# Kernel tuning notes

Measured on AMD Instinct MI355X. Metric: run time of the kernel, lower is better.

The kernel has to match this reference:

```python
import jax, jax.numpy as jnp
import numpy as np

B, C, H, N = 2, 128, 128, 2048   # batch, in_channels, hidden_dim, points per view
TEMP = 0.1
ITERS = 20
EPS = 1e-8


def setup_inputs() -> dict:
    key = jax.random.key(0)
    ks = jax.random.split(key, 4)
    s = lambda fan_in: 1.0 / np.sqrt(fan_in)
    return {
        "feat_d": jax.random.normal(ks[0], (B, C, N), jnp.float32),
        "feat_s": jax.random.normal(ks[1], (B, C, N), jnp.float32),
        # dustbin_head params: Conv1d(C->H, k=1) -> ReLU -> Conv1d(H->1, k=1)
        "W1": jax.random.normal(ks[2], (H, C), jnp.float32) * s(C),
        "b1": jnp.zeros((H,), jnp.float32),
        "W2": jax.random.normal(ks[3], (1, H), jnp.float32) * s(H),
        "b2": jnp.zeros((1,), jnp.float32),
    }


def _dustbin_head(x, W1, b1, W2, b2):
    # 1x1 Conv1d == channel matmul. x: [B, C, N] -> [B, 1, N]
    h = jax.nn.relu(jnp.einsum('hc,bcn->bhn', W1, x) + b1[None, :, None])
    return jnp.einsum('oh,bhn->bon', W2, h) + b2[None, :, None]


def _log_cross_view_ot(feat_q, feat_k, dustbin, temperature, iters):
    # scores: [B, Nq, Nk]; dustbin appended as the last row -> [B, Nq+1, Nk]
    scores = jnp.einsum('bcn,bcm->bnm', feat_q, feat_k) / temperature
    log_T0 = jnp.concatenate([scores, dustbin], axis=1)

    def step(log_T, _):
        log_T = log_T - jax.nn.logsumexp(log_T, axis=2, keepdims=True)  # row norm
        log_T = log_T - jax.nn.logsumexp(log_T, axis=1, keepdims=True)  # col norm
        return log_T, None

    log_T, _ = jax.lax.scan(step, log_T0, None, length=iters)
    return log_T


def reference(feat_d, feat_s, W1, b1, W2, b2):
    # N_d == N_s, so the torch F.interpolate calls are identity ops.
    dust_d = _dustbin_head(feat_d, W1, b1, W2, b2)  # [B, 1, N]
    dust_s = _dustbin_head(feat_s, W1, b1, W2, b2)  # [B, 1, N]

    log_T_ds = _log_cross_view_ot(feat_d, feat_s, dust_d, TEMP, ITERS)
    log_T_sd = _log_cross_view_ot(feat_s, feat_d, dust_s, TEMP, ITERS)

    T_ds = jnp.exp(log_T_ds[:, :-1, :])  # drop dustbin row -> [B, N, N]
    T_sd = jnp.exp(log_T_sd[:, :-1, :])

    loss_consistency = jnp.mean((T_ds - jnp.swapaxes(T_sd, 1, 2)) ** 2)

    entropy_ds = -(T_ds * jnp.log(T_ds + EPS)).sum(axis=(1, 2)).mean()
    entropy_sd = -(T_sd * jnp.log(T_sd + EPS)).sum(axis=(1, 2)).mean()
    loss_entropy = 0.5 * (entropy_ds + entropy_sd)

    return loss_consistency + 0.01 * loss_entropy
```

## Files before the change

kernel.cpp:

```cpp
#include <hip/hip_runtime.h>
#include <hip/hip_fp16.h>
#include <math.h>

#define NPTS 2048
#define NB 2
#define NC 128
#define NH 128
#define INV_TEMP 10.0f
#define NITERS 20
#define EPSF 1e-8f

static __device__ __forceinline__ void lse_merge(float& m, float& s, float m2, float s2){
  float M = fmaxf(m, m2);
  s = s * __expf(m - M) + s2 * __expf(m2 - M);
  m = M;
}

static __device__ __forceinline__ void unpack8(uint4 raw, float* x){
  float2 f;
  f = __half22float2(*(__half2*)&raw.x); x[0]=f.x; x[1]=f.y;
  f = __half22float2(*(((__half2*)&raw.x)+1)); x[2]=f.x; x[3]=f.y;
  f = __half22float2(*(__half2*)&raw.z); x[4]=f.x; x[5]=f.y;
  f = __half22float2(*(((__half2*)&raw.z)+1)); x[6]=f.x; x[7]=f.y;
}

static __device__ __forceinline__ float reduce32_lse(float* x){
  float mt[16];
  #pragma unroll
  for (int i = 0; i < 16; ++i) mt[i] = fmaxf(x[i], x[i + 16]);
  #pragma unroll
  for (int st = 8; st >= 1; st >>= 1)
    #pragma unroll
    for (int i = 0; i < 8; ++i) if (i < st) mt[i] = fmaxf(mt[i], mt[i + st]);
  float m = mt[0];
  float s0 = 0.f, s1 = 0.f, s2 = 0.f, s3 = 0.f;
  #pragma unroll
  for (int i = 0; i < 32; i += 4){
    s0 += __expf(x[i]     - m);
    s1 += __expf(x[i + 1] - m);
    s2 += __expf(x[i + 2] - m);
    s3 += __expf(x[i + 3] - m);
  }
  float s = (s0 + s1) + (s2 + s3);
  #pragma unroll
  for (int d = 1; d < 64; d <<= 1){
    float m2 = __shfl_xor(m, d);
    float sx = __shfl_xor(s, d);
    lse_merge(m, s, m2, sx);
  }
  return m + __logf(s);
}

__global__ __launch_bounds__(128) void dust_kernel(
    const float* __restrict__ fd, const float* __restrict__ fs,
    const float* __restrict__ W1, const float* __restrict__ b1,
    const float* __restrict__ W2, const float* __restrict__ b2,
    float* __restrict__ dust_d, float* __restrict__ dust_s){
  const int chunk = blockIdx.x, b = blockIdx.y, view = blockIdx.z;
  const float* x = (view == 0 ? fd : fs) + (size_t)b * NC * NPTS;
  float* out = (view == 0 ? dust_d : dust_s) + (size_t)b * NPTS;
  const int n0 = chunk * 16;
  __shared__ float xs[NC][17];
  __shared__ float red[NH][17];
  const int j = threadIdx.x;
  #pragma unroll
  for (int p = 0; p < 16; ++p) xs[j][p] = x[(size_t)j * NPTS + n0 + p];
  __syncthreads();
  float acc[16];
  float bb = b1[j];
  #pragma unroll
  for (int p = 0; p < 16; ++p) acc[p] = bb;
  for (int c = 0; c < NC; ++c){
    float w = W1[j * NC + c];
    #pragma unroll
    for (int p = 0; p < 16; ++p) acc[p] = fmaf(w, xs[c][p], acc[p]);
  }
  float w2 = W2[j];
  #pragma unroll
  for (int p = 0; p < 16; ++p) red[j][p] = w2 * fmaxf(acc[p], 0.0f);
  __syncthreads();
  for (int s = NH / 2; s >= 1; s >>= 1){
    if (j < s){
      #pragma unroll
      for (int p = 0; p < 16; ++p) red[j][p] += red[j + s][p];
    }
    __syncthreads();
  }
  if (j < 16) out[n0 + j] = red[0][j] + b2[0];
}

#define GP 68
#define KC 64
__global__ __launch_bounds__(256) void gemm_kernel(
    const float* __restrict__ fd, const float* __restrict__ fs,
    __half* __restrict__ S, __half* __restrict__ ST){
  const int cb = blockIdx.x, rb = blockIdx.y, b = blockIdx.z;
  const float* A = fd + (size_t)b * NC * NPTS;
  const float* Bm = fs + (size_t)b * NC * NPTS;
  __shared__ float Als[KC * GP];
  __shared__ float Bls[KC * GP];
  const int tid = threadIdx.x;
  const int tx = tid & 15, ty = tid >> 4;
  float acc[4][4] = {};
  for (int kc = 0; kc < NC; kc += KC){
    for (int idx = tid; idx < KC * 64; idx += 256){
      int ch = idx >> 6, i = idx & 63;
      Als[ch * GP + i] = A[(size_t)(kc + ch) * NPTS + rb * 64 + i];
      Bls[ch * GP + i] = Bm[(size_t)(kc + ch) * NPTS + cb * 64 + i];
    }
    __syncthreads();
    for (int c = 0; c < KC; ++c){
      float4 a4 = *(const float4*)&Als[c * GP + ty * 4];
      float4 b4 = *(const float4*)&Bls[c * GP + tx * 4];
      float av[4] = {a4.x, a4.y, a4.z, a4.w};
      float bv[4] = {b4.x, b4.y, b4.z, b4.w};
      #pragma unroll
      for (int i = 0; i < 4; ++i)
        #pragma unroll
        for (int jj = 0; jj < 4; ++jj)
          acc[i][jj] = fmaf(av[i], bv[jj], acc[i][jj]);
    }
    __syncthreads();
  }
  __half* Sb = S + (size_t)b * NPTS * NPTS;
  __half* STb = ST + (size_t)b * NPTS * NPTS;
  const int r0 = rb * 64 + ty * 4, c0 = cb * 64 + tx * 4;
  #pragma unroll
  for (int i = 0; i < 4; ++i){
    __half2 p[2];
    p[0] = __float22half2_rn(make_float2(acc[i][0]*INV_TEMP, acc[i][1]*INV_TEMP));
    p[1] = __float22half2_rn(make_float2(acc[i][2]*INV_TEMP, acc[i][3]*INV_TEMP));
    *(uint2*)&Sb[(size_t)(r0 + i) * NPTS + c0] = *(uint2*)p;
  }
  #pragma unroll
  for (int jj = 0; jj < 4; ++jj){
    __half2 p[2];
    p[0] = __float22half2_rn(make_float2(acc[0][jj]*INV_TEMP, acc[1][jj]*INV_TEMP));
    p[1] = __float22half2_rn(make_float2(acc[2][jj]*INV_TEMP, acc[3][jj]*INV_TEMP));
    *(uint2*)&STb[(size_t)(c0 + jj) * NPTS + r0] = *(uint2*)p;
  }
}

__global__ __launch_bounds__(512, 4) void phase_kernel(
    const __half* __restrict__ S, const __half* __restrict__ ST,
    const float* __restrict__ dust_d, const float* __restrict__ dust_s,
    float* __restrict__ u_ds, float* __restrict__ u_sd,
    float* __restrict__ v_ds, float* __restrict__ v_sd,
    const int mode){
  const int b = blockIdx.y, mat = blockIdx.z;
  const int w = threadIdx.x >> 6, lane = threadIdx.x & 63;
  const int r = blockIdx.x * 8 + w;
  const int rmax = (mode == 0) ? (NPTS + 1) : NPTS;
  if (blockIdx.x * 8 >= rmax) return;

  __shared__ float lds_off[NPTS];
  {
    const float* off;
    if (mode == 0) off = (mat == 0 ? v_ds : v_sd) + b * NPTS;
    else           off = (mat == 0 ? u_sd : u_ds) + b * (NPTS + 1);
    *(float4*)&lds_off[threadIdx.x * 4] = *(const float4*)&off[threadIdx.x * 4];
  }
  __syncthreads();

  if (r >= rmax) return;

  float x[32];
  if (mode == 0 && r == NPTS){
    const float* drow = (mat == 0 ? dust_d : dust_s) + b * NPTS;
    #pragma unroll
    for (int k = 0; k < 8; ++k){
      const int c = (k * 64 + lane) * 4;
      float4 rv = *(const float4*)&drow[c];
      float4 o  = *(const float4*)&lds_off[c];
      x[k*4+0]=rv.x+o.x; x[k*4+1]=rv.y+o.y; x[k*4+2]=rv.z+o.z; x[k*4+3]=rv.w+o.w;
    }
  } else {
    const __half* row = (mat == 0 ? S : ST) + ((size_t)b * NPTS + r) * NPTS;
    #pragma unroll
    for (int k2 = 0; k2 < 4; ++k2){
      const int c = (k2 * 64 + lane) * 8;
      uint4 raw = *(const uint4*)&row[c];
      float xr[8];
      unpack8(raw, xr);
      float4 o0 = *(const float4*)&lds_off[c];
      float4 o1 = *(const float4*)&lds_off[c + 4];
      x[k2*8+0]=xr[0]+o0.x; x[k2*8+1]=xr[1]+o0.y; x[k2*8+2]=xr[2]+o0.z; x[k2*8+3]=xr[3]+o0.w;
      x[k2*8+4]=xr[4]+o1.x; x[k2*8+5]=xr[5]+o1.y; x[k2*8+6]=xr[6]+o1.z; x[k2*8+7]=xr[7]+o1.w;
    }
  }

  float lse = reduce32_lse(x);
  if (lane == 0){
    if (mode == 0){
      (mat == 0 ? u_ds : u_sd)[b * (NPTS + 1) + r] = -lse;
    } else {
      float dsc = (mat == 0 ? dust_s : dust_d)[b * NPTS + r];
      float uN  = (mat == 0 ? u_sd : u_ds)[b * (NPTS + 1) + NPTS];
      float e = dsc + uN;
      float M2 = fmaxf(lse, e);
      lse = M2 + __logf(__expf(lse - M2) + __expf(e - M2));
      (mat == 0 ? v_sd : v_ds)[b * NPTS + r] = -lse;
    }
  }
}

__global__ __launch_bounds__(512, 4) void loss_kernel(
    const __half* __restrict__ S,
    const float* __restrict__ u_ds, const float* __restrict__ u_sd,
    const float* __restrict__ v_ds, const float* __restrict__ v_sd,
    float* __restrict__ part){
  const int b = blockIdx.y;
  const int w = threadIdx.x >> 6, lane = threadIdx.x & 63;
  const int r = blockIdx.x * 8 + w;

  __shared__ float lds_vds[NPTS];
  __shared__ float lds_usd[NPTS];
  *(float4*)&lds_vds[threadIdx.x * 4] = *(const float4*)&v_ds[b * NPTS + threadIdx.x * 4];
  *(float4*)&lds_usd[threadIdx.x * 4] = *(const float4*)&u_sd[b * (NPTS + 1) + threadIdx.x * 4];
  __syncthreads();

  const __half* row = S + ((size_t)b * NPTS + r) * NPTS;
  const float uds = u_ds[b * (NPTS + 1) + r];
  const float vsd = v_sd[b * NPTS + r];
  float sd = 0.f, e1 = 0.f, e2 = 0.f;
  #pragma unroll
  for (int k2 = 0; k2 < 4; ++k2){
    const int c = (k2 * 64 + lane) * 8;
    uint4 raw = *(const uint4*)&row[c];
    float sv[8];
    unpack8(raw, sv);
    float4 a0 = *(const float4*)&lds_vds[c];
    float4 a1 = *(const float4*)&lds_vds[c + 4];
    float4 q0 = *(const float4*)&lds_usd[c];
    float4 q1 = *(const float4*)&lds_usd[c + 4];
    float av[8] = {a0.x,a0.y,a0.z,a0.w,a1.x,a1.y,a1.z,a1.w};
    float qv[8] = {q0.x,q0.y,q0.z,q0.w,q1.x,q1.y,q1.z,q1.w};
    #pragma unroll
    for (int i = 0; i < 8; ++i){
      float t1 = __expf(sv[i] + uds + av[i]);
      float t2 = __expf(sv[i] + qv[i] + vsd);
      float d = t1 - t2;
      sd += d * d;
      e1 += t1 * __logf(t1 + EPSF);
      e2 += t2 * __logf(t2 + EPSF);
    }
  }
  #pragma unroll
  for (int d = 1; d < 64; d <<= 1){
    sd += __shfl_xor(sd, d);
    e1 += __shfl_xor(e1, d);
    e2 += __shfl_xor(e2, d);
  }
  if (lane == 0){
    float* p = part + ((size_t)b * NPTS + r) * 4;
    p[0] = sd; p[1] = e1; p[2] = e2;
  }
}

__global__ __launch_bounds__(256) void final_kernel(const float* __restrict__ part, float* __restrict__ out){
  const int tid = threadIdx.x;
  float s0 = 0.f, s1 = 0.f, s2 = 0.f;
  for (int i = tid; i < NB * NPTS; i += 256){
    s0 += part[(size_t)i * 4 + 0];
    s1 += part[(size_t)i * 4 + 1];
    s2 += part[(size_t)i * 4 + 2];
  }
  #pragma unroll
  for (int d = 1; d < 64; d <<= 1){
    s0 += __shfl_xor(s0, d);
    s1 += __shfl_xor(s1, d);
    s2 += __shfl_xor(s2, d);
  }
  __shared__ float rs[4][3];
  const int w = tid >> 6;
  if ((tid & 63) == 0){ rs[w][0] = s0; rs[w][1] = s1; rs[w][2] = s2; }
  __syncthreads();
  if (tid == 0){
    float a0 = rs[0][0] + rs[1][0] + rs[2][0] + rs[3][0];
    float a1 = rs[0][1] + rs[1][1] + rs[2][1] + rs[3][1];
    float a2 = rs[0][2] + rs[1][2] + rs[2][2] + rs[3][2];
    float lc = a0 / (float)((size_t)NB * NPTS * NPTS);
    float le = -0.5f * (a1 + a2) / (float)NB;
    out[0] = lc + 0.01f * le;
  }
}

extern "C" void kernel_launch(void* const* d_in, const int* in_sizes, int n_in,
                              void* d_out, int out_size, void* d_ws, size_t ws_size,
                              hipStream_t stream){
  const float* fd = (const float*)d_in[0];
  const float* fs = (const float*)d_in[1];
  const float* W1 = (const float*)d_in[2];
  const float* b1 = (const float*)d_in[3];
  const float* W2 = (const float*)d_in[4];
  const float* b2 = (const float*)d_in[5];
  char* ws = (char*)d_ws;
  __half* S  = (__half*)ws;
  __half* ST = S + (size_t)NB * NPTS * NPTS;
  float* fws = (float*)(ws + 2 * sizeof(__half) * (size_t)NB * NPTS * NPTS);
  float* dust_d = fws;
  float* dust_s = dust_d + (size_t)NB * NPTS;
  float* u_ds   = dust_s + (size_t)NB * NPTS;
  float* u_sd   = u_ds + (size_t)NB * (NPTS + 1);
  float* v_ds   = u_sd + (size_t)NB * (NPTS + 1);
  float* v_sd   = v_ds + (size_t)NB * NPTS;
  float* part   = v_sd + (size_t)NB * NPTS;

  hipMemsetAsync(v_ds, 0, sizeof(float) * (size_t)NB * NPTS * 2, stream);

  dust_kernel<<<dim3(NPTS / 16, NB, 2), 128, 0, stream>>>(fd, fs, W1, b1, W2, b2, dust_d, dust_s);
  gemm_kernel<<<dim3(NPTS / 64, NPTS / 64, NB), 256, 0, stream>>>(fd, fs, S, ST);
  const dim3 pgrid((NPTS + 1 + 7) / 8, NB, 2);
  for (int it = 0; it < NITERS; ++it){
    phase_kernel<<<pgrid, 512, 0, stream>>>(S, ST, dust_d, dust_s, u_ds, u_sd, v_ds, v_sd, 0);
    phase_kernel<<<pgrid, 512, 0, stream>>>(S, ST, dust_d, dust_s, u_ds, u_sd, v_ds, v_sd, 1);
  }
  loss_kernel<<<dim3(NPTS / 8, NB), 512, 0, stream>>>(S, u_ds, u_sd, v_ds, v_sd, part);
  final_kernel<<<1, 256, 0, stream>>>(part, (float*)d_out);
}
```

Before: 395.9 us.

## Drop transposed score matrix; compute transposed-view LSE via column reduction

Stops writing the transposed half-precision score matrix ST. The second OT problem's row log-sum-exp is now computed as a two-pass (max then sum-exp) column reduction over S, using dedicated column blocks that run alongside the row blocks in one launch. This halves workspace and GEMM store traffic, and removes the strided transposed writes. In exchange the column path reads S twice per phase and does more exps. The loss kernel also replaces log(t+eps) with the pre-exp argument, dropping a log per element at a tiny numerical difference from the epsilon.

```diff
diff --git a/kernel.cpp b/kernel.cpp
--- a/kernel.cpp
+++ b/kernel.cpp
@@ -9,6 +9,7 @@
 #define INV_TEMP 10.0f
 #define NITERS 20
 #define EPSF 1e-8f
+#define NEGINF -3.0e38f
 
 static __device__ __forceinline__ void lse_merge(float& m, float& s, float m2, float s2){
   float M = fmaxf(m, m2);
@@ -93,7 +94,7 @@
 #define KC 64
 __global__ __launch_bounds__(256) void gemm_kernel(
     const float* __restrict__ fd, const float* __restrict__ fs,
-    __half* __restrict__ S, __half* __restrict__ ST){
+    __half* __restrict__ S){
   const int cb = blockIdx.x, rb = blockIdx.y, b = blockIdx.z;
   const float* A = fd + (size_t)b * NC * NPTS;
   const float* Bm = fs + (size_t)b * NC * NPTS;
@@ -123,7 +124,6 @@
     __syncthreads();
   }
   __half* Sb = S + (size_t)b * NPTS * NPTS;
-  __half* STb = ST + (size_t)b * NPTS * NPTS;
   const int r0 = rb * 64 + ty * 4, c0 = cb * 64 + tx * 4;
   #pragma unroll
   for (int i = 0; i < 4; ++i){
@@ -132,74 +132,174 @@
     p[1] = __float22half2_rn(make_float2(acc[i][2]*INV_TEMP, acc[i][3]*INV_TEMP));
     *(uint2*)&Sb[(size_t)(r0 + i) * NPTS + c0] = *(uint2*)p;
   }
-  #pragma unroll
-  for (int jj = 0; jj < 4; ++jj){
-    __half2 p[2];
-    p[0] = __float22half2_rn(make_float2(acc[0][jj]*INV_TEMP, acc[1][jj]*INV_TEMP));
-    p[1] = __float22half2_rn(make_float2(acc[2][jj]*INV_TEMP, acc[3][jj]*INV_TEMP));
-    *(uint2*)&STb[(size_t)(c0 + jj) * NPTS + r0] = *(uint2*)p;
-  }
-}
-
+}
+
+#define NCOLBLK (NB * 32)
+#define NROWBLK (NB * 257)
 __global__ __launch_bounds__(512, 4) void phase_kernel(
-    const __half* __restrict__ S, const __half* __restrict__ ST,
+    const __half* __restrict__ S,
     const float* __restrict__ dust_d, const float* __restrict__ dust_s,
     float* __restrict__ u_ds, float* __restrict__ u_sd,
     float* __restrict__ v_ds, float* __restrict__ v_sd,
     const int mode){
-  const int b = blockIdx.y, mat = blockIdx.z;
-  const int w = threadIdx.x >> 6, lane = threadIdx.x & 63;
-  const int r = blockIdx.x * 8 + w;
-  const int rmax = (mode == 0) ? (NPTS + 1) : NPTS;
-  if (blockIdx.x * 8 >= rmax) return;
+  const int tid = threadIdx.x;
+
+  if (blockIdx.x < NCOLBLK){
+    const int b  = blockIdx.x >> 5;
+    const int j0 = (blockIdx.x & 31) * 64;
+    const __half* Sb = S + (size_t)b * NPTS * NPTS;
+    __shared__ float lds_off[NPTS];
+    __shared__ float mbuf[8 * 64];
+    __shared__ float maxfin[64];
+    __shared__ float sbuf[8 * 64];
+    {
+      const float* roff = (mode == 0 ? v_sd + b * NPTS : u_ds + b * (NPTS + 1));
+      *(float4*)&lds_off[tid * 4] = *(const float4*)&roff[tid * 4];
+    }
+    __syncthreads();
+
+    const int ss = tid & 7;
+    const int g  = tid >> 3;
+    const int w  = tid >> 6, lane = tid & 63;
+    const size_t base = (size_t)j0 + (size_t)ss * 8;
+
+    float m[8];
+    #pragma unroll
+    for (int i = 0; i < 8; ++i) m[i] = NEGINF;
+    for (int rnd = 0; rnd < 32; ++rnd){
+      const int r = rnd * 64 + g;
+      uint4 raw = *(const uint4*)&Sb[(size_t)r * NPTS + base];
+      float off = lds_off[r];
+      float xv[8];
+      unpack8(raw, xv);
+      #pragma unroll
+      for (int i = 0; i < 8; ++i) m[i] = fmaxf(m[i], xv[i] + off);
+    }
+    #pragma unroll
+    for (int d = 8; d < 64; d <<= 1)
+      #pragma unroll
+      for (int i = 0; i < 8; ++i) m[i] = fmaxf(m[i], __shfl_xor(m[i], d));
+    if (lane < 8){
+      #pragma unroll
+      for (int i = 0; i < 8; ++i) mbuf[w * 64 + lane * 8 + i] = m[i];
+    }
+    __syncthreads();
+    if (tid < 64){
+      float mf = mbuf[tid];
+      #pragma unroll
+      for (int ww = 1; ww < 8; ++ww) mf = fmaxf(mf, mbuf[ww * 64 + tid]);
+      maxfin[tid] = mf;
+    }
+    __syncthreads();
+
+    float ref[8], s[8];
+    #pragma unroll
+    for (int i = 0; i < 8; ++i){ ref[i] = maxfin[ss * 8 + i]; s[i] = 0.f; }
+    for (int rnd = 0; rnd < 32; ++rnd){
+      const int r = rnd * 64 + g;
+      uint4 raw = *(const uint4*)&Sb[(size_t)r * NPTS + base];
+      float off = lds_off[r];
+      float xv[8];
+      unpack8(raw, xv);
+      #pragma unroll
+      for (int i = 0; i < 8; ++i) s[i] += __expf(xv[i] + off - ref[i]);
+    }
+    #pragma unroll
+    for (int d = 8; d < 64; d <<= 1)
+      #pragma unroll
+      for (int i = 0; i < 8; ++i) s[i] += __shfl_xor(s[i], d);
+    if (lane < 8){
+      #pragma unroll
+      for (int i = 0; i < 8; ++i) sbuf[w * 64 + lane * 8 + i] = s[i];
+    }
+    __syncthreads();
+    if (tid < 64){
+      float sf = sbuf[tid];
+      #pragma unroll
+      for (int ww = 1; ww < 8; ++ww) sf += sbuf[ww * 64 + tid];
+      float lse = maxfin[tid] + __logf(sf);
+      const int j = j0 + tid;
+      if (mode == 0){
+        u_sd[b * (NPTS + 1) + j] = -lse;
+      } else {
+        float e = dust_d[b * NPTS + j] + u_ds[b * (NPTS + 1) + NPTS];
+        float M2 = fmaxf(lse, e);
+        lse = M2 + __logf(__expf(lse - M2) + __expf(e - M2));
+        v_ds[b * NPTS + j] = -lse;
+      }
+    }
+    return;
+  }
+
+  const int id = blockIdx.x - NCOLBLK;
+  const int b = id & 1;
+  const int rbx = id >> 1;
+  const int w = tid >> 6, lane = tid & 63;
+  const int r = rbx * 8 + w;
 
   __shared__ float lds_off[NPTS];
   {
-    const float* off;
-    if (mode == 0) off = (mat == 0 ? v_ds : v_sd) + b * NPTS;
-    else           off = (mat == 0 ? u_sd : u_ds) + b * (NPTS + 1);
-    *(float4*)&lds_off[threadIdx.x * 4] = *(const float4*)&off[threadIdx.x * 4];
+    const float* off = (mode == 0 ? v_ds + b * NPTS : u_sd + b * (NPTS + 1));
+    *(float4*)&lds_off[tid * 4] = *(const float4*)&off[tid * 4];
   }
   __syncthreads();
 
-  if (r >= rmax) return;
-
-  float x[32];
-  if (mode == 0 && r == NPTS){
-    const float* drow = (mat == 0 ? dust_d : dust_s) + b * NPTS;
-    #pragma unroll
-    for (int k = 0; k < 8; ++k){
-      const int c = (k * 64 + lane) * 4;
-      float4 rv = *(const float4*)&drow[c];
-      float4 o  = *(const float4*)&lds_off[c];
-      x[k*4+0]=rv.x+o.x; x[k*4+1]=rv.y+o.y; x[k*4+2]=rv.z+o.z; x[k*4+3]=rv.w+o.w;
+  if (mode == 0){
+    if (r < NPTS){
+      const __half* row = S + ((size_t)b * NPTS + r) * NPTS;
+      float x[32];
+      #pragma unroll
+      for (int k2 = 0; k2 < 4; ++k2){
+        const int c = (k2 * 64 + lane) * 8;
+        uint4 raw = *(const uint4*)&row[c];
+        float xr[8];
+        unpack8(raw, xr);
+        float4 o0 = *(const float4*)&lds_off[c];
+        float4 o1 = *(const float4*)&lds_off[c + 4];
+        x[k2*8+0]=xr[0]+o0.x; x[k2*8+1]=xr[1]+o0.y; x[k2*8+2]=xr[2]+o0.z; x[k2*8+3]=xr[3]+o0.w;
+        x[k2*8+4]=xr[4]+o1.x; x[k2*8+5]=xr[5]+o1.y; x[k2*8+6]=xr[6]+o1.z; x[k2*8+7]=xr[7]+o1.w;
+      }
+      float lse = reduce32_lse(x);
+      if (lane == 0) u_ds[b * (NPTS + 1) + r] = -lse;
+    } else if (r == NPTS || r == NPTS + 1){
+      const float* drow = (r == NPTS ? dust_d : dust_s) + b * NPTS;
+      const float* offg = v_sd + b * NPTS;
+      float x[32];
+      #pragma unroll
+      for (int k = 0; k < 8; ++k){
+        const int c = (k * 64 + lane) * 4;
+        float4 rv = *(const float4*)&drow[c];
+        float4 o = (r == NPTS) ? *(const float4*)&lds_off[c] : *(const float4*)&offg[c];
+        x[k*4+0]=rv.x+o.x; x[k*4+1]=rv.y+o.y; x[k*4+2]=rv.z+o.z; x[k*4+3]=rv.w+o.w;
+      }
+      float lse = reduce32_lse(x);
+      if (lane == 0){
+        if (r == NPTS) u_ds[b * (NPTS + 1) + NPTS] = -lse;
+        else           u_sd[b * (NPTS + 1) + NPTS] = -lse;
+      }
     }
   } else {
-    const __half* row = (mat == 0 ? S : ST) + ((size_t)b * NPTS + r) * NPTS;
-    #pragma unroll
-    for (int k2 = 0; k2 < 4; ++k2){
-      const int c = (k2 * 64 + lane) * 8;
-      uint4 raw = *(const uint4*)&row[c];
-      float xr[8];
-      unpack8(raw, xr);
-      float4 o0 = *(const float4*)&lds_off[c];
-      float4 o1 = *(const float4*)&lds_off[c + 4];
-      x[k2*8+0]=xr[0]+o0.x; x[k2*8+1]=xr[1]+o0.y; x[k2*8+2]=xr[2]+o0.z; x[k2*8+3]=xr[3]+o0.w;
-      x[k2*8+4]=xr[4]+o1.x; x[k2*8+5]=xr[5]+o1.y; x[k2*8+6]=xr[6]+o1.z; x[k2*8+7]=xr[7]+o1.w;
-    }
-  }
-
-  float lse = reduce32_lse(x);
-  if (lane == 0){
-    if (mode == 0){
-      (mat == 0 ? u_ds : u_sd)[b * (NPTS + 1) + r] = -lse;
-    } else {
-      float dsc = (mat == 0 ? dust_s : dust_d)[b * NPTS + r];
-      float uN  = (mat == 0 ? u_sd : u_ds)[b * (NPTS + 1) + NPTS];
-      float e = dsc + uN;
-      float M2 = fmaxf(lse, e);
-      lse = M2 + __logf(__expf(lse - M2) + __expf(e - M2));
-      (mat == 0 ? v_sd : v_ds)[b * NPTS + r] = -lse;
+    if (r < NPTS){
+      const __half* row = S + ((size_t)b * NPTS + r) * NPTS;
+      float x[32];
+      #pragma unroll
+      for (int k2 = 0; k2 < 4; ++k2){
+        const int c = (k2 * 64 + lane) * 8;
+        uint4 raw = *(const uint4*)&row[c];
+        float xr[8];
+        unpack8(raw, xr);
+        float4 o0 = *(const float4*)&lds_off[c];
+        float4 o1 = *(const float4*)&lds_off[c + 4];
+        x[k2*8+0]=xr[0]+o0.x; x[k2*8+1]=xr[1]+o0.y; x[k2*8+2]=xr[2]+o0.z; x[k2*8+3]=xr[3]+o0.w;
+        x[k2*8+4]=xr[4]+o1.x; x[k2*8+5]=xr[5]+o1.y; x[k2*8+6]=xr[6]+o1.z; x[k2*8+7]=xr[7]+o1.w;
+      }
+      float lse = reduce32_lse(x);
+      if (lane == 0){
+        float e = dust_s[b * NPTS + r] + u_sd[b * (NPTS + 1) + NPTS];
+        float M2 = fmaxf(lse, e);
+        lse = M2 + __logf(__expf(lse - M2) + __expf(e - M2));
+        v_sd[b * NPTS + r] = -lse;
+      }
     }
   }
 }
@@ -237,12 +337,14 @@
     float qv[8] = {q0.x,q0.y,q0.z,q0.w,q1.x,q1.y,q1.z,q1.w};
     #pragma unroll
     for (int i = 0; i < 8; ++i){
-      float t1 = __expf(sv[i] + uds + av[i]);
-      float t2 = __expf(sv[i] + qv[i] + vsd);
+      float y1 = sv[i] + uds + av[i];
+      float y2 = sv[i] + qv[i] + vsd;
+      float t1 = __expf(y1);
+      float t2 = __expf(y2);
       float d = t1 - t2;
       sd += d * d;
-      e1 += t1 * __logf(t1 + EPSF);
-      e2 += t2 * __logf(t2 + EPSF);
+      e1 += t1 * y1;
+      e2 += t2 * y2;
     }
   }
   #pragma unroll
@@ -295,9 +397,8 @@
   const float* W2 = (const float*)d_in[4];
   const float* b2 = (const float*)d_in[5];
   char* ws = (char*)d_ws;
-  __half* S  = (__half*)ws;
-  __half* ST = S + (size_t)NB * NPTS * NPTS;
-  float* fws = (float*)(ws + 2 * sizeof(__half) * (size_t)NB * NPTS * NPTS);
+  __half* S = (__half*)ws;
+  float* fws = (float*)(ws + sizeof(__half) * (size_t)NB * NPTS * NPTS);
   float* dust_d = fws;
   float* dust_s = dust_d + (size_t)NB * NPTS;
   float* u_ds   = dust_s + (size_t)NB * NPTS;
@@ -309,11 +410,10 @@
   hipMemsetAsync(v_ds, 0, sizeof(float) * (size_t)NB * NPTS * 2, stream);
 
   dust_kernel<<<dim3(NPTS / 16, NB, 2), 128, 0, stream>>>(fd, fs, W1, b1, W2, b2, dust_d, dust_s);
-  gemm_kernel<<<dim3(NPTS / 64, NPTS / 64, NB), 256, 0, stream>>>(fd, fs, S, ST);
-  const dim3 pgrid((NPTS + 1 + 7) / 8, NB, 2);
+  gemm_kernel<<<dim3(NPTS / 64, NPTS / 64, NB), 256, 0, stream>>>(fd, fs, S);
   for (int it = 0; it < NITERS; ++it){
-    phase_kernel<<<pgrid, 512, 0, stream>>>(S, ST, dust_d, dust_s, u_ds, u_sd, v_ds, v_sd, 0);
-    phase_kernel<<<pgrid, 512, 0, stream>>>(S, ST, dust_d, dust_s, u_ds, u_sd, v_ds, v_sd, 1);
+    phase_kernel<<<NCOLBLK + NROWBLK, 512, 0, stream>>>(S, dust_d, dust_s, u_ds, u_sd, v_ds, v_sd, 0);
+    phase_kernel<<<NCOLBLK + NROWBLK, 512, 0, stream>>>(S, dust_d, dust_s, u_ds, u_sd, v_ds, v_sd, 1);
   }
   loss_kernel<<<dim3(NPTS / 8, NB), 512, 0, stream>>>(S, u_ds, u_sd, v_ds, v_sd, part);
   final_kernel<<<1, 256, 0, stream>>>(part, (float*)d_out);
```

After: 694.9 us. +75.5%, slower.
